# Optimization experiments

Hardware: AMD Instinct MI355X
Metric: run time of the kernel (lower is better)

Reference implementation:

```python
import jax, jax.numpy as jnp
import numpy as np

T, B = 128, 256          # frames, batch (free dims)
C_IN = 201               # in_features
KD = 3                   # keypoint_dimensionality
NK = C_IN // KD          # 67 keypoints = attention seq len
E = 8                    # d_pose_embed
H = 2                    # heads
DH = E // H              # head dim = 4
L = 12                   # encoder layers
FF = 2 * E               # 16
OUT = 128                # output_size
EPS = 1e-5


def setup_inputs() -> dict:
    key = jax.random.key(0)
    ks = jax.random.split(key, 12)
    s = 0.1
    return {
        "pose_clip": jax.random.normal(ks[0], (T, B, C_IN), jnp.float32),
        "embed_w": jax.random.normal(ks[1], (E, KD), jnp.float32) * s,
        "embed_b": jax.random.normal(ks[2], (E,), jnp.float32) * s,
        "in_proj_w": jax.random.normal(ks[3], (L, 3 * E, E), jnp.float32) * s,
        "in_proj_b": jax.random.normal(ks[4], (L, 3 * E), jnp.float32) * s,
        "attn_out_w": jax.random.normal(ks[5], (L, E, E), jnp.float32) * s,
        "attn_out_b": jax.random.normal(ks[6], (L, E), jnp.float32) * s,
        "ff1_w": jax.random.normal(ks[7], (L, FF, E), jnp.float32) * s,
        "ff1_b": jax.random.normal(ks[8], (L, FF), jnp.float32) * s,
        "ff2_w": jax.random.normal(ks[9], (L, E, FF), jnp.float32) * s,
        "ff2_b": jax.random.normal(ks[10], (L, E), jnp.float32) * s,
        "ln1_g": jnp.ones((L, E), jnp.float32),
        "ln1_b": jnp.zeros((L, E), jnp.float32),
        "ln2_g": jnp.ones((L, E), jnp.float32),
        "ln2_b": jnp.zeros((L, E), jnp.float32),
        "out_w": jax.random.normal(ks[11], (OUT, NK * E), jnp.float32) * s,
        "out_b": jnp.zeros((OUT,), jnp.float32),
    }


def _ln(x, g, b):
    m = jnp.mean(x, axis=-1, keepdims=True)
    v = jnp.mean(jnp.square(x - m), axis=-1, keepdims=True)
    return (x - m) * jax.lax.rsqrt(v + EPS) * g + b


def _encoder(x, layer_params):
    # x: [S, N, E]; post-LN TransformerEncoderLayer, relu activation, no dropout (eval)
    def step(h, p):
        ipw, ipb, aow, aob, f1w, f1b, f2w, f2b, g1, b1, g2, b2 = p
        S, N, _ = h.shape
        qkv = h @ ipw.T + ipb                      # [S, N, 3E]
        q, k, v = jnp.split(qkv, 3, axis=-1)
        q = q.reshape(S, N, H, DH)
        k = k.reshape(S, N, H, DH)
        v = v.reshape(S, N, H, DH)
        scores = jnp.einsum('snhd,tnhd->nhst', q, k) / np.sqrt(DH).astype(h.dtype)
        attn = jax.nn.softmax(scores, axis=-1)
        o = jnp.einsum('nhst,tnhd->snhd', attn, v).reshape(S, N, E)
        o = o @ aow.T + aob
        h = _ln(h + o, g1, b1)
        ff = jax.nn.relu(h @ f1w.T + f1b) @ f2w.T + f2b
        h = _ln(h + ff, g2, b2)
        return h, None
    x, _ = jax.lax.scan(step, x, layer_params)
    return x


def reference(pose_clip, embed_w, embed_b, in_proj_w, in_proj_b, attn_out_w,
              attn_out_b, ff1_w, ff1_b, ff2_w, ff2_b, ln1_g, ln1_b, ln2_g,
              ln2_b, out_w, out_b):
    t, b, c = pose_clip.shape
    nk = c // KD
    # [t,b,c] -> [t*b, nk, 3] -> [nk, t*b, 3]  (seq=keypoints, batch=t*b)
    x = pose_clip.reshape(t * b, nk, KD).transpose(1, 0, 2)
    x = x @ embed_w.T + embed_b                    # [nk, t*b, E]
    layer_params = (in_proj_w, in_proj_b, attn_out_w, attn_out_b,
                    ff1_w, ff1_b, ff2_w, ff2_b, ln1_g, ln1_b, ln2_g, ln2_b)
    x = _encoder(x, layer_params)
    x = x.transpose(1, 0, 2).reshape(t, b, nk * E)  # [t, b, 536]
    return jnp.tanh(x @ out_w.T + out_b)            # [t, b, 128]
```

## Files before the change

kernel.cpp:

```cpp
#include <hip/hip_runtime.h>
#include <math.h>

#define NTOT 32768
#define CIN  201
#define S    67
#define E    8
#define H    2
#define L    12
#define FF   16
#define OUTC 128
#define KF   536
#define EPB  7
#define LPE  34
#define THREADS 256
#define NPAIR 34

typedef float v2f __attribute__((ext_vector_type(2)));

#if __has_builtin(__builtin_amdgcn_exp2f)
#define EXP2F(x) __builtin_amdgcn_exp2f(x)
#else
#define EXP2F(x) exp2f(x)
#endif
#if __has_builtin(__builtin_amdgcn_rcpf)
#define RCPF(x) __builtin_amdgcn_rcpf(x)
#else
#define RCPF(x) (1.0f/(x))
#endif
#if __has_builtin(__builtin_amdgcn_rsqf)
#define RSQF(x) __builtin_amdgcn_rsqf(x)
#else
#define RSQF(x) rsqrtf(x)
#endif

#define QSCALE 0.7213475204444817f

__device__ __forceinline__ v2f sp(float x) { return (v2f){x, x}; }

__device__ __forceinline__ void ln8p(v2f* x, const float* __restrict__ gg,
                                     const float* __restrict__ bb) {
    v2f m = {0.f, 0.f};
    #pragma unroll
    for (int e = 0; e < E; ++e) m += x[e];
    m *= 0.125f;
    v2f v = {0.f, 0.f};
    #pragma unroll
    for (int e = 0; e < E; ++e) { v2f d = x[e] - m; v += d * d; }
    v *= 0.125f;
    v2f rs;
    rs.x = RSQF(v.x + 1e-5f);
    rs.y = RSQF(v.y + 1e-5f);
    #pragma unroll
    for (int e = 0; e < E; ++e) x[e] = (x[e] - m) * rs * sp(gg[e]) + sp(bb[e]);
}

__global__ __launch_bounds__(THREADS, 5)
void enc_kernel(const float* __restrict__ pose,
                const float* __restrict__ ew,  const float* __restrict__ ebias,
                const float* __restrict__ ipw, const float* __restrict__ ipb,
                const float* __restrict__ aow, const float* __restrict__ aob,
                const float* __restrict__ f1w, const float* __restrict__ f1b,
                const float* __restrict__ f2w, const float* __restrict__ f2b,
                const float* __restrict__ g1,  const float* __restrict__ b1,
                const float* __restrict__ g2,  const float* __restrict__ b2,
                float* __restrict__ xf)
{
    __shared__ float4 KA[EPB * H][NPAIR];
    __shared__ float4 KB[EPB * H][NPAIR];
    __shared__ float4 VA[EPB * H][NPAIR];
    __shared__ float4 VB[EPB * H][NPAIR];

    const int lid = threadIdx.x;
    const int g   = lid / LPE;
    const int j   = lid - g * LPE;
    const int n   = blockIdx.x * EPB + g;
    const bool active = (g < EPB) && (n < NTOT);
    const bool pad = (j == LPE - 1);
    const int r0 = 2 * j;

    v2f xr[E];
    if (active) {
        const float* p0 = pose + (size_t)n * CIN + 3 * r0;
        const float* p1 = pad ? p0 : (p0 + 3);
        v2f c0 = {p0[0], p1[0]};
        v2f c1 = {p0[1], p1[1]};
        v2f c2 = {p0[2], p1[2]};
        #pragma unroll
        for (int e = 0; e < E; ++e)
            xr[e] = sp(ebias[e]) + c0 * sp(ew[e*3+0]) + c1 * sp(ew[e*3+1])
                                 + c2 * sp(ew[e*3+2]);
    }

    #pragma unroll 1
    for (int l = 0; l < L; ++l) {
        const float* W  = ipw + l * 192;
        const float* Bq = ipb + l * 24;

        v2f qp[E];
        if (active) {
            v2f qkv[24];
            #pragma unroll
            for (int jo = 0; jo < 24; ++jo) {
                v2f a = sp(Bq[jo]);
                #pragma unroll
                for (int e = 0; e < E; ++e) a += xr[e] * sp(W[jo*8 + e]);
                qkv[jo] = a;
            }
            #pragma unroll
            for (int c = 0; c < E; ++c) qp[c] = qkv[c] * QSCALE;
            if (pad) {
                #pragma unroll
                for (int c = 8; c < 24; ++c) qkv[c].y = 0.f;
            }
            #pragma unroll
            for (int h = 0; h < H; ++h) {
                const int gh = g*2 + h;
                KA[gh][j] = make_float4(qkv[8+4*h+0].x, qkv[8+4*h+0].y,
                                        qkv[8+4*h+1].x, qkv[8+4*h+1].y);
                KB[gh][j] = make_float4(qkv[8+4*h+2].x, qkv[8+4*h+2].y,
                                        qkv[8+4*h+3].x, qkv[8+4*h+3].y);
                VA[gh][j] = make_float4(qkv[16+4*h+0].x, qkv[16+4*h+0].y,
                                        qkv[16+4*h+1].x, qkv[16+4*h+1].y);
                VB[gh][j] = make_float4(qkv[16+4*h+2].x, qkv[16+4*h+2].y,
                                        qkv[16+4*h+3].x, qkv[16+4*h+3].y);
            }
        }
        __syncthreads();

        if (active) {
            v2f os[E];
            #pragma unroll
            for (int h = 0; h < H; ++h) {
                const int gh = g*2 + h;
                const float4* pKA = KA[gh];
                const float4* pKB = KB[gh];
                const float4* pVA = VA[gh];
                const float4* pVB = VB[gh];
                const v2f q0l = sp(qp[4*h+0].x), q0h = sp(qp[4*h+0].y);
                const v2f q1l = sp(qp[4*h+1].x), q1h = sp(qp[4*h+1].y);
                const v2f q2l = sp(qp[4*h+2].x), q2h = sp(qp[4*h+2].y);
                const v2f q3l = sp(qp[4*h+3].x), q3h = sp(qp[4*h+3].y);
                v2f ls0 = {0.f,0.f}, ls1 = {0.f,0.f};
                v2f oc00={0.f,0.f}, oc01={0.f,0.f}, oc02={0.f,0.f}, oc03={0.f,0.f};
                v2f oc10={0.f,0.f}, oc11={0.f,0.f}, oc12={0.f,0.f}, oc13={0.f,0.f};
                #pragma unroll
                for (int i = 0; i < NPAIR; ++i) {
                    float4 ka = pKA[i], kb = pKB[i];
                    float4 va = pVA[i], vb = pVB[i];
                    v2f kx = *(const v2f*)&ka.x, ky = *(const v2f*)&ka.z;
                    v2f kz = *(const v2f*)&kb.x, kw = *(const v2f*)&kb.z;
                    v2f sc0 = q0l*kx + q1l*ky + q2l*kz + q3l*kw;
                    v2f sc1 = q0h*kx + q1h*ky + q2h*kz + q3h*kw;
                    v2f e0, e1;
                    e0.x = EXP2F(sc0.x);  e0.y = EXP2F(sc0.y);
                    e1.x = EXP2F(sc1.x);  e1.y = EXP2F(sc1.y);
                    ls0 += e0;  ls1 += e1;
                    v2f v0 = *(const v2f*)&va.x, v1 = *(const v2f*)&va.z;
                    v2f v2 = *(const v2f*)&vb.x, v3 = *(const v2f*)&vb.z;
                    oc00 += e0*v0; oc01 += e0*v1; oc02 += e0*v2; oc03 += e0*v3;
                    oc10 += e1*v0; oc11 += e1*v1; oc12 += e1*v2; oc13 += e1*v3;
                }
                float l0 = ls0.x + ls0.y - 1.0f;
                float l1 = ls1.x + ls1.y - 1.0f;
                float i0 = RCPF(l0), i1 = RCPF(l1);
                os[4*h+0] = (v2f){(oc00.x+oc00.y)*i0, (oc10.x+oc10.y)*i1};
                os[4*h+1] = (v2f){(oc01.x+oc01.y)*i0, (oc11.x+oc11.y)*i1};
                os[4*h+2] = (v2f){(oc02.x+oc02.y)*i0, (oc12.x+oc12.y)*i1};
                os[4*h+3] = (v2f){(oc03.x+oc03.y)*i0, (oc13.x+oc13.y)*i1};
            }

            {
                const float* WA = aow + l*64;
                const float* BA = aob + l*8;
                #pragma unroll
                for (int e = 0; e < E; ++e) {
                    v2f a = sp(BA[e]);
                    #pragma unroll
                    for (int e2 = 0; e2 < E; ++e2) a += os[e2] * sp(WA[e*8 + e2]);
                    xr[e] += a;
                }
            }
            ln8p(xr, g1 + l*E, b1 + l*E);

            {
                const float* W1 = f1w + l*128;
                const float* B1 = f1b + l*16;
                const float* W2 = f2w + l*128;
                const float* B2 = f2b + l*8;
                v2f t1[FF];
                #pragma unroll
                for (int f = 0; f < FF; ++f) {
                    v2f a = sp(B1[f]);
                    #pragma unroll
                    for (int e = 0; e < E; ++e) a += xr[e] * sp(W1[f*8 + e]);
                    a.x = fmaxf(a.x, 0.f);
                    a.y = fmaxf(a.y, 0.f);
                    t1[f] = a;
                }
                #pragma unroll
                for (int e = 0; e < E; ++e) {
                    v2f a = sp(B2[e]);
                    #pragma unroll
                    for (int f = 0; f < FF; ++f) a += t1[f] * sp(W2[e*16 + f]);
                    xr[e] += a;
                }
            }
            ln8p(xr, g2 + l*E, b2 + l*E);
        }
        __syncthreads();
    }

    if (active) {
        float* dst = xf + (size_t)n * KF + r0 * E;
        *(float4*)(dst + 0) = make_float4(xr[0].x, xr[1].x, xr[2].x, xr[3].x);
        *(float4*)(dst + 4) = make_float4(xr[4].x, xr[5].x, xr[6].x, xr[7].x);
        if (!pad) {
            *(float4*)(dst + 8)  = make_float4(xr[0].y, xr[1].y, xr[2].y, xr[3].y);
            *(float4*)(dst + 12) = make_float4(xr[4].y, xr[5].y, xr[6].y, xr[7].y);
        }
    }
}

__global__ void tr_kernel(const float* __restrict__ ow, float* __restrict__ wt)
{
    int i = blockIdx.x * 256 + threadIdx.x;
    if (i < OUTC * KF) {
        int c = i / KF, k = i - c * KF;
        wt[k * OUTC + c] = ow[i];
    }
}

__global__ __launch_bounds__(256, 4)
void out_kernel(const float* __restrict__ xf, const float* __restrict__ wt,
                const float* __restrict__ ob, float* __restrict__ out)
{
    __shared__ float Xs[32][68];
    const int lid = threadIdx.x;
    const int tx  = lid & 31;
    const int ty  = lid >> 5;
    const int n0  = blockIdx.x * 32;

    float acc[4][4] = {};

    #pragma unroll 1
    for (int kc = 0; kc < 9; ++kc) {
        const int kb = kc * 64;
        const int kw = (kc < 8) ? 64 : 24;
        __syncthreads();
        const int nvec = 32 * (kw >> 2);
        for (int i = lid; i < nvec; i += 256) {
            int r = i / (kw >> 2), kq = i - r * (kw >> 2);
            *(float4*)&Xs[r][kq*4] =
                *(const float4*)&xf[(size_t)(n0 + r) * KF + kb + kq*4];
        }
        __syncthreads();
        #pragma unroll 4
        for (int k = 0; k < kw; ++k) {
            float4 w4 = *(const float4*)&wt[(size_t)(kb + k) * OUTC + tx*4];
            #pragma unroll
            for (int i = 0; i < 4; ++i) {
                float x = Xs[ty*4 + i][k];
                acc[i][0] += x*w4.x; acc[i][1] += x*w4.y;
                acc[i][2] += x*w4.z; acc[i][3] += x*w4.w;
            }
        }
    }

    const float4 bb = *(const float4*)&ob[tx*4];
    #pragma unroll
    for (int i = 0; i < 4; ++i) {
        int r = n0 + ty*4 + i;
        float4 v;
        v.x = tanhf(acc[i][0] + bb.x);
        v.y = tanhf(acc[i][1] + bb.y);
        v.z = tanhf(acc[i][2] + bb.z);
        v.w = tanhf(acc[i][3] + bb.w);
        *(float4*)(out + (size_t)r * OUTC + tx*4) = v;
    }
}

extern "C" void kernel_launch(void* const* d_in, const int* in_sizes, int n_in,
                              void* d_out, int out_size, void* d_ws, size_t ws_size,
                              hipStream_t stream) {
    (void)in_sizes; (void)n_in; (void)out_size; (void)ws_size;
    const float* pose = (const float*)d_in[0];
    const float* ew   = (const float*)d_in[1];
    const float* eb   = (const float*)d_in[2];
    const float* ipw  = (const float*)d_in[3];
    const float* ipb  = (const float*)d_in[4];
    const float* aow  = (const float*)d_in[5];
    const float* aob  = (const float*)d_in[6];
    const float* f1w  = (const float*)d_in[7];
    const float* f1b  = (const float*)d_in[8];
    const float* f2w  = (const float*)d_in[9];
    const float* f2b  = (const float*)d_in[10];
    const float* g1   = (const float*)d_in[11];
    const float* b1   = (const float*)d_in[12];
    const float* g2   = (const float*)d_in[13];
    const float* b2   = (const float*)d_in[14];
    const float* ow   = (const float*)d_in[15];
    const float* ob   = (const float*)d_in[16];

    float* xf = (float*)d_ws;
    float* wt = xf + (size_t)NTOT * KF;

    const int grid1 = (NTOT + EPB - 1) / EPB;
    enc_kernel<<<grid1, THREADS, 0, stream>>>(pose, ew, eb, ipw, ipb, aow, aob,
                                              f1w, f1b, f2w, f2b, g1, b1, g2, b2, xf);
    tr_kernel<<<(OUTC*KF + 255)/256, 256, 0, stream>>>(ow, wt);
    out_kernel<<<NTOT / 32, 256, 0, stream>>>(xf, wt, ob, (float*)d_out);
}
```

Measured before the change: 1.324 ms.

## Use fp16 packed dot2 for encoder matmuls and attention with fp16 K/V in LDS

Encoder weights are pre-converted to packed fp16 pairs by a new prep kernel. All small matmuls (QKV, out-proj, FFN) and the attention score and value accumulation now use v_dot2 fp16 instructions with fp32 accumulation, so each instruction covers two multiply-adds. K/V are stored in LDS as packed halves, which halves shared-memory footprint and read traffic, and the occupancy hint is raised to 6 blocks. Precision drops to fp16 for activations, exp values and weights, which risks accuracy across 12 layers.

```diff
diff --git a/kernel.cpp b/kernel.cpp
--- a/kernel.cpp
+++ b/kernel.cpp
@@ -16,6 +16,8 @@
 #define NPAIR 34
 
 typedef float v2f __attribute__((ext_vector_type(2)));
+typedef _Float16 v2h __attribute__((ext_vector_type(2)));
+typedef __fp16   v2hf __attribute__((ext_vector_type(2)));
 
 #if __has_builtin(__builtin_amdgcn_exp2f)
 #define EXP2F(x) __builtin_amdgcn_exp2f(x)
@@ -32,10 +34,27 @@
 #else
 #define RSQF(x) rsqrtf(x)
 #endif
+#if __has_builtin(__builtin_amdgcn_fdot2)
+#define FDOT2(a,b,c) __builtin_amdgcn_fdot2((a),(b),(c),false)
+#else
+#define FDOT2(a,b,c) ((float)(a).x*(float)(b).x + (float)(a).y*(float)(b).y + (c))
+#endif
+
+static __device__ __forceinline__ v2h CVTPK(float a, float b) {
+#if __has_builtin(__builtin_amdgcn_cvt_pkrtz)
+    union { v2hf f; v2h h; } x;
+    x.f = __builtin_amdgcn_cvt_pkrtz(a, b);
+    return x.h;
+#else
+    return (v2h){(_Float16)a, (_Float16)b};
+#endif
+}
 
 #define QSCALE 0.7213475204444817f
 
 __device__ __forceinline__ v2f sp(float x) { return (v2f){x, x}; }
+__device__ __forceinline__ unsigned int h2u(v2h h){ union{v2h h;unsigned int u;}x; x.h=h; return x.u; }
+__device__ __forceinline__ v2h u2h(unsigned int u){ union{unsigned int u;v2h h;}x; x.u=u; return x.h; }
 
 __device__ __forceinline__ void ln8p(v2f* x, const float* __restrict__ gg,
                                      const float* __restrict__ bb) {
@@ -54,21 +73,33 @@
     for (int e = 0; e < E; ++e) x[e] = (x[e] - m) * rs * sp(gg[e]) + sp(bb[e]);
 }
 
-__global__ __launch_bounds__(THREADS, 5)
+__global__ void prep_kernel(const float* __restrict__ ipw, const float* __restrict__ aow,
+                            const float* __restrict__ f1w, const float* __restrict__ f2w,
+                            unsigned int* __restrict__ wph)
+{
+    int idx = blockIdx.x * 256 + threadIdx.x;
+    if (idx >= L * 256) return;
+    int l = idx >> 8, r = idx & 255;
+    float a, b;
+    if (r < 96)       { int j = r >> 2, p = r & 3; a = ipw[l*192 + j*8 + 2*p]; b = ipw[l*192 + j*8 + 2*p+1]; }
+    else if (r < 128) { int q = r - 96;  int e = q >> 2, p = q & 3; a = aow[l*64 + e*8 + 2*p]; b = aow[l*64 + e*8 + 2*p+1]; }
+    else if (r < 192) { int q = r - 128; int f = q >> 2, p = q & 3; a = f1w[l*128 + f*8 + 2*p]; b = f1w[l*128 + f*8 + 2*p+1]; }
+    else              { int q = r - 192; int e = q >> 3, p = q & 7; a = f2w[l*128 + e*16 + 2*p]; b = f2w[l*128 + e*16 + 2*p+1]; }
+    wph[idx] = h2u(CVTPK(a, b));
+}
+
+__global__ __launch_bounds__(THREADS, 6)
 void enc_kernel(const float* __restrict__ pose,
                 const float* __restrict__ ew,  const float* __restrict__ ebias,
-                const float* __restrict__ ipw, const float* __restrict__ ipb,
-                const float* __restrict__ aow, const float* __restrict__ aob,
-                const float* __restrict__ f1w, const float* __restrict__ f1b,
-                const float* __restrict__ f2w, const float* __restrict__ f2b,
+                const unsigned int* __restrict__ wph, const float* __restrict__ ipb,
+                const float* __restrict__ aob,
+                const float* __restrict__ f1b, const float* __restrict__ f2b,
                 const float* __restrict__ g1,  const float* __restrict__ b1,
                 const float* __restrict__ g2,  const float* __restrict__ b2,
                 float* __restrict__ xf)
 {
-    __shared__ float4 KA[EPB * H][NPAIR];
-    __shared__ float4 KB[EPB * H][NPAIR];
-    __shared__ float4 VA[EPB * H][NPAIR];
-    __shared__ float4 VB[EPB * H][NPAIR];
+    __shared__ uint4 KHs[EPB * H][NPAIR];
+    __shared__ uint4 VHs[EPB * H][NPAIR];
 
     const int lid = threadIdx.x;
     const int g   = lid / LPE;
@@ -77,6 +108,8 @@
     const bool active = (g < EPB) && (n < NTOT);
     const bool pad = (j == LPE - 1);
     const int r0 = 2 * j;
+
+    const v2h one2 = {(_Float16)1.0f, (_Float16)1.0f};
 
     v2f xr[E];
     if (active) {
@@ -93,116 +126,166 @@
 
     #pragma unroll 1
     for (int l = 0; l < L; ++l) {
-        const float* W  = ipw + l * 192;
+        const unsigned int* WL = wph + l * 256;
+        const v2h* qkvh = (const v2h*)WL;
+        const v2h* aowh = (const v2h*)(WL + 96);
+        const v2h* f1h  = (const v2h*)(WL + 128);
+        const v2h* f2h  = (const v2h*)(WL + 192);
         const float* Bq = ipb + l * 24;
 
-        v2f qp[E];
+        v2h qh[H][2][2];
         if (active) {
-            v2f qkv[24];
-            #pragma unroll
-            for (int jo = 0; jo < 24; ++jo) {
-                v2f a = sp(Bq[jo]);
-                #pragma unroll
-                for (int e = 0; e < E; ++e) a += xr[e] * sp(W[jo*8 + e]);
-                qkv[jo] = a;
-            }
-            #pragma unroll
-            for (int c = 0; c < E; ++c) qp[c] = qkv[c] * QSCALE;
-            if (pad) {
-                #pragma unroll
-                for (int c = 8; c < 24; ++c) qkv[c].y = 0.f;
-            }
+            v2h xh0[4], xh1[4];
+            #pragma unroll
+            for (int p = 0; p < 4; ++p) {
+                xh0[p] = CVTPK(xr[2*p].x, xr[2*p+1].x);
+                xh1[p] = CVTPK(xr[2*p].y, xr[2*p+1].y);
+            }
+            #pragma unroll
+            for (int c = 0; c < 4; ++c) {
+                float a0b = Bq[2*c], a1b = Bq[2*c+1];
+                float q0a = a0b, q0b = a1b, q1a = a0b, q1b = a1b;
+                #pragma unroll
+                for (int p = 0; p < 4; ++p) {
+                    q0a = FDOT2(xh0[p], qkvh[(2*c)*4 + p], q0a);
+                    q0b = FDOT2(xh0[p], qkvh[(2*c+1)*4 + p], q0b);
+                    q1a = FDOT2(xh1[p], qkvh[(2*c)*4 + p], q1a);
+                    q1b = FDOT2(xh1[p], qkvh[(2*c+1)*4 + p], q1b);
+                }
+                const int h = c >> 1, d = (c & 1) ? 1 : 0;
+                qh[h][0][d] = CVTPK(q0a * QSCALE, q0b * QSCALE);
+                qh[h][1][d] = CVTPK(q1a * QSCALE, q1b * QSCALE);
+            }
+            #pragma unroll
+            for (int h = 0; h < H; ++h) {
+                float k0[4], k1[4], v0[4], v1[4];
+                #pragma unroll
+                for (int d = 0; d < 4; ++d) {
+                    const int jk = 8 + 4*h + d, jv = 16 + 4*h + d;
+                    float ak0 = Bq[jk], ak1 = Bq[jk];
+                    float av0 = Bq[jv], av1 = Bq[jv];
+                    #pragma unroll
+                    for (int p = 0; p < 4; ++p) {
+                        ak0 = FDOT2(xh0[p], qkvh[jk*4 + p], ak0);
+                        ak1 = FDOT2(xh1[p], qkvh[jk*4 + p], ak1);
+                        av0 = FDOT2(xh0[p], qkvh[jv*4 + p], av0);
+                        av1 = FDOT2(xh1[p], qkvh[jv*4 + p], av1);
+                    }
+                    k0[d] = ak0; k1[d] = ak1; v0[d] = av0; v1[d] = av1;
+                }
+                if (pad) {
+                    #pragma unroll
+                    for (int d = 0; d < 4; ++d) { k1[d] = 0.f; v1[d] = 0.f; }
+                }
+                const int gh = g*2 + h;
+                KHs[gh][j] = make_uint4(h2u(CVTPK(k0[0], k0[1])), h2u(CVTPK(k0[2], k0[3])),
+                                        h2u(CVTPK(k1[0], k1[1])), h2u(CVTPK(k1[2], k1[3])));
+                VHs[gh][j] = make_uint4(h2u(CVTPK(v0[0], v1[0])), h2u(CVTPK(v0[1], v1[1])),
+                                        h2u(CVTPK(v0[2], v1[2])), h2u(CVTPK(v0[3], v1[3])));
+            }
+        }
+        __syncthreads();
+
+        if (active) {
+            float on0[E], on1[E];
             #pragma unroll
             for (int h = 0; h < H; ++h) {
                 const int gh = g*2 + h;
-                KA[gh][j] = make_float4(qkv[8+4*h+0].x, qkv[8+4*h+0].y,
-                                        qkv[8+4*h+1].x, qkv[8+4*h+1].y);
-                KB[gh][j] = make_float4(qkv[8+4*h+2].x, qkv[8+4*h+2].y,
-                                        qkv[8+4*h+3].x, qkv[8+4*h+3].y);
-                VA[gh][j] = make_float4(qkv[16+4*h+0].x, qkv[16+4*h+0].y,
-                                        qkv[16+4*h+1].x, qkv[16+4*h+1].y);
-                VB[gh][j] = make_float4(qkv[16+4*h+2].x, qkv[16+4*h+2].y,
-                                        qkv[16+4*h+3].x, qkv[16+4*h+3].y);
-            }
-        }
-        __syncthreads();
-
-        if (active) {
-            v2f os[E];
-            #pragma unroll
-            for (int h = 0; h < H; ++h) {
-                const int gh = g*2 + h;
-                const float4* pKA = KA[gh];
-                const float4* pKB = KB[gh];
-                const float4* pVA = VA[gh];
-                const float4* pVB = VB[gh];
-                const v2f q0l = sp(qp[4*h+0].x), q0h = sp(qp[4*h+0].y);
-                const v2f q1l = sp(qp[4*h+1].x), q1h = sp(qp[4*h+1].y);
-                const v2f q2l = sp(qp[4*h+2].x), q2h = sp(qp[4*h+2].y);
-                const v2f q3l = sp(qp[4*h+3].x), q3h = sp(qp[4*h+3].y);
-                v2f ls0 = {0.f,0.f}, ls1 = {0.f,0.f};
-                v2f oc00={0.f,0.f}, oc01={0.f,0.f}, oc02={0.f,0.f}, oc03={0.f,0.f};
-                v2f oc10={0.f,0.f}, oc11={0.f,0.f}, oc12={0.f,0.f}, oc13={0.f,0.f};
+                const uint4* pK = KHs[gh];
+                const uint4* pV = VHs[gh];
+                const v2h qA0 = qh[h][0][0], qB0 = qh[h][0][1];
+                const v2h qA1 = qh[h][1][0], qB1 = qh[h][1][1];
+                float ls0 = 0.f, ls1 = 0.f;
+                float o00=0.f,o01=0.f,o02=0.f,o03=0.f;
+                float o10=0.f,o11=0.f,o12=0.f,o13=0.f;
                 #pragma unroll
                 for (int i = 0; i < NPAIR; ++i) {
-                    float4 ka = pKA[i], kb = pKB[i];
-                    float4 va = pVA[i], vb = pVB[i];
-                    v2f kx = *(const v2f*)&ka.x, ky = *(const v2f*)&ka.z;
-                    v2f kz = *(const v2f*)&kb.x, kw = *(const v2f*)&kb.z;
-                    v2f sc0 = q0l*kx + q1l*ky + q2l*kz + q3l*kw;
-                    v2f sc1 = q0h*kx + q1h*ky + q2h*kz + q3h*kw;
-                    v2f e0, e1;
-                    e0.x = EXP2F(sc0.x);  e0.y = EXP2F(sc0.y);
-                    e1.x = EXP2F(sc1.x);  e1.y = EXP2F(sc1.y);
-                    ls0 += e0;  ls1 += e1;
-                    v2f v0 = *(const v2f*)&va.x, v1 = *(const v2f*)&va.z;
-                    v2f v2 = *(const v2f*)&vb.x, v3 = *(const v2f*)&vb.z;
-                    oc00 += e0*v0; oc01 += e0*v1; oc02 += e0*v2; oc03 += e0*v3;
-                    oc10 += e1*v0; oc11 += e1*v1; oc12 += e1*v2; oc13 += e1*v3;
-                }
-                float l0 = ls0.x + ls0.y - 1.0f;
-                float l1 = ls1.x + ls1.y - 1.0f;
-                float i0 = RCPF(l0), i1 = RCPF(l1);
-                os[4*h+0] = (v2f){(oc00.x+oc00.y)*i0, (oc10.x+oc10.y)*i1};
-                os[4*h+1] = (v2f){(oc01.x+oc01.y)*i0, (oc11.x+oc11.y)*i1};
-                os[4*h+2] = (v2f){(oc02.x+oc02.y)*i0, (oc12.x+oc12.y)*i1};
-                os[4*h+3] = (v2f){(oc03.x+oc03.y)*i0, (oc13.x+oc13.y)*i1};
+                    uint4 kk = pK[i];
+                    uint4 vv = pV[i];
+                    float s00 = FDOT2(qA0, u2h(kk.x), FDOT2(qB0, u2h(kk.y), 0.f));
+                    float s01 = FDOT2(qA0, u2h(kk.z), FDOT2(qB0, u2h(kk.w), 0.f));
+                    float s10 = FDOT2(qA1, u2h(kk.x), FDOT2(qB1, u2h(kk.y), 0.f));
+                    float s11 = FDOT2(qA1, u2h(kk.z), FDOT2(qB1, u2h(kk.w), 0.f));
+                    float e00 = EXP2F(s00), e01 = EXP2F(s01);
+                    float e10 = EXP2F(s10), e11 = EXP2F(s11);
+                    v2h ep0 = CVTPK(e00, e01);
+                    v2h ep1 = CVTPK(e10, e11);
+                    ls0 = FDOT2(ep0, one2, ls0);
+                    ls1 = FDOT2(ep1, one2, ls1);
+                    o00 = FDOT2(ep0, u2h(vv.x), o00);
+                    o01 = FDOT2(ep0, u2h(vv.y), o01);
+                    o02 = FDOT2(ep0, u2h(vv.z), o02);
+                    o03 = FDOT2(ep0, u2h(vv.w), o03);
+                    o10 = FDOT2(ep1, u2h(vv.x), o10);
+                    o11 = FDOT2(ep1, u2h(vv.y), o11);
+                    o12 = FDOT2(ep1, u2h(vv.z), o12);
+                    o13 = FDOT2(ep1, u2h(vv.w), o13);
+                }
+                float i0 = RCPF(ls0 - 1.0f);
+                float i1 = RCPF(ls1 - 1.0f);
+                on0[4*h+0] = o00*i0; on0[4*h+1] = o01*i0;
+                on0[4*h+2] = o02*i0; on0[4*h+3] = o03*i0;
+                on1[4*h+0] = o10*i1; on1[4*h+1] = o11*i1;
+                on1[4*h+2] = o12*i1; on1[4*h+3] = o13*i1;
             }
 
             {
-                const float* WA = aow + l*64;
-                const float* BA = aob + l*8;
+                const float* BA = aob + l*E;
+                v2h oh0[4], oh1[4];
+                #pragma unroll
+                for (int p = 0; p < 4; ++p) {
+                    oh0[p] = CVTPK(on0[2*p], on0[2*p+1]);
+                    oh1[p] = CVTPK(on1[2*p], on1[2*p+1]);
+                }
                 #pragma unroll
                 for (int e = 0; e < E; ++e) {
-                    v2f a = sp(BA[e]);
-                    #pragma unroll
-                    for (int e2 = 0; e2 < E; ++e2) a += os[e2] * sp(WA[e*8 + e2]);
-                    xr[e] += a;
+                    float a0 = BA[e], a1 = BA[e];
+                    #pragma unroll
+                    for (int p = 0; p < 4; ++p) {
+                        a0 = FDOT2(oh0[p], aowh[e*4 + p], a0);
+                        a1 = FDOT2(oh1[p], aowh[e*4 + p], a1);
+                    }
+                    xr[e] += (v2f){a0, a1};
                 }
             }
             ln8p(xr, g1 + l*E, b1 + l*E);
 
             {
-                const float* W1 = f1w + l*128;
-                const float* B1 = f1b + l*16;
-                const float* W2 = f2w + l*128;
-                const float* B2 = f2b + l*8;
-                v2f t1[FF];
+                const float* B1 = f1b + l*FF;
+                const float* B2 = f2b + l*E;
+                v2h xh0[4], xh1[4];
+                #pragma unroll
+                for (int p = 0; p < 4; ++p) {
+                    xh0[p] = CVTPK(xr[2*p].x, xr[2*p+1].x);
+                    xh1[p] = CVTPK(xr[2*p].y, xr[2*p+1].y);
+                }
+                float t0[FF], t1v[FF];
                 #pragma unroll
                 for (int f = 0; f < FF; ++f) {
-                    v2f a = sp(B1[f]);
-                    #pragma unroll
-                    for (int e = 0; e < E; ++e) a += xr[e] * sp(W1[f*8 + e]);
-                    a.x = fmaxf(a.x, 0.f);
-                    a.y = fmaxf(a.y, 0.f);
-                    t1[f] = a;
+                    float a0 = B1[f], a1 = B1[f];
+                    #pragma unroll
+                    for (int p = 0; p < 4; ++p) {
+                        a0 = FDOT2(xh0[p], f1h[f*4 + p], a0);
+                        a1 = FDOT2(xh1[p], f1h[f*4 + p], a1);
+                    }
+                    t0[f] = fmaxf(a0, 0.f);
+                    t1v[f] = fmaxf(a1, 0.f);
+                }
+                v2h th0[8], th1[8];
+                #pragma unroll
+                for (int p = 0; p < 8; ++p) {
+                    th0[p] = CVTPK(t0[2*p], t0[2*p+1]);
+                    th1[p] = CVTPK(t1v[2*p], t1v[2*p+1]);
                 }
                 #pragma unroll
                 for (int e = 0; e < E; ++e) {
-                    v2f a = sp(B2[e]);
-                    #pragma unroll
-                    for (int f = 0; f < FF; ++f) a += t1[f] * sp(W2[e*16 + f]);
-                    xr[e] += a;
+                    float a0 = B2[e], a1 = B2[e];
+                    #pragma unroll
+                    for (int p = 0; p < 8; ++p) {
+                        a0 = FDOT2(th0[p], f2h[e*8 + p], a0);
+                        a1 = FDOT2(th1[p], f2h[e*8 + p], a1);
+                    }
+                    xr[e] += (v2f){a0, a1};
                 }
             }
             ln8p(xr, g2 + l*E, b2 + l*E);
@@ -303,10 +386,12 @@
 
     float* xf = (float*)d_ws;
     float* wt = xf + (size_t)NTOT * KF;
-
+    unsigned int* wph = (unsigned int*)(wt + (size_t)KF * OUTC);
+
+    prep_kernel<<<(L*256 + 255)/256, 256, 0, stream>>>(ipw, aow, f1w, f2w, wph);
     const int grid1 = (NTOT + EPB - 1) / EPB;
-    enc_kernel<<<grid1, THREADS, 0, stream>>>(pose, ew, eb, ipw, ipb, aow, aob,
-                                              f1w, f1b, f2w, f2b, g1, b1, g2, b2, xf);
+    enc_kernel<<<grid1, THREADS, 0, stream>>>(pose, ew, eb, wph, ipb, aob,
+                                              f1b, f2b, g1, b1, g2, b2, xf);
     tr_kernel<<<(OUTC*KF + 255)/256, 256, 0, stream>>>(ow, wt);
     out_kernel<<<NTOT / 32, 256, 0, stream>>>(xf, wt, ob, (float*)d_out);
 }
```

New measurement: 1.402 ms. 5.9% more time.
